# Optimization experiments

Hardware: AMD Instinct MI355X
Metric: run time of the kernel (lower is better)

The kernel has to match this reference:

```python
import jax, jax.numpy as jnp
import numpy as np

X_DIM, Z_DIM, H, B, T = 257, 16, 128, 256, 512


def _p(key, shape, scale=0.05):
    return jax.random.normal(key, shape, jnp.float32) * scale


def setup_inputs() -> dict:
    key = jax.random.key(0)
    ks = jax.random.split(key, 16)
    z4 = jnp.zeros((4 * H,), jnp.float32)
    return {
        "x": jax.random.uniform(ks[0], (B, X_DIM, T), jnp.float32),
        "eps": jax.random.normal(ks[1], (T, B, Z_DIM), jnp.float32),
        # rnn_g_x: backward LSTM over x
        "Wih_gx": _p(ks[2], (4 * H, X_DIM)), "Whh_gx": _p(ks[3], (4 * H, H)),
        "bih_gx": z4, "bhh_gx": z4,
        # rnn_g_z: forward LSTM cell over sampled z
        "Wih_gz": _p(ks[4], (4 * H, Z_DIM)), "Whh_gz": _p(ks[5], (4 * H, H)),
        "bih_gz": z4, "bhh_gz": z4,
        # mlp_inference (one dense layer, tanh) + heads
        "W0": _p(ks[6], (H, 2 * H)), "b0": jnp.zeros((H,), jnp.float32),
        "Wm": _p(ks[7], (Z_DIM, H)), "bm": jnp.zeros((Z_DIM,), jnp.float32),
        "Wv": _p(ks[8], (Z_DIM, H)), "bv": jnp.zeros((Z_DIM,), jnp.float32),
        # decoder rnn_h + gen_logvar
        "Wih_h": _p(ks[9], (4 * H, Z_DIM)), "Whh_h": _p(ks[10], (4 * H, H)),
        "bih_h": z4, "bhh_h": z4,
        "Wy": _p(ks[11], (X_DIM, H)), "by": jnp.zeros((X_DIM,), jnp.float32),
    }


def _lstm(xs, Wih, Whh, b, reverse=False):
    # xs: (T, B, in); single-layer LSTM, PyTorch gate order i,f,g,o
    Bn, Hd = xs.shape[1], Whh.shape[1]

    def step(carry, x_t):
        h, c = carry
        g = x_t @ Wih.T + h @ Whh.T + b
        i, f, gg, o = jnp.split(g, 4, axis=-1)
        c = jax.nn.sigmoid(f) * c + jax.nn.sigmoid(i) * jnp.tanh(gg)
        h = jax.nn.sigmoid(o) * jnp.tanh(c)
        return (h, c), h

    init = (jnp.zeros((Bn, Hd), xs.dtype), jnp.zeros((Bn, Hd), xs.dtype))
    _, hs = jax.lax.scan(step, init, xs, reverse=reverse)
    return hs


def reference(x, eps, Wih_gx, Whh_gx, bih_gx, bhh_gx,
              Wih_gz, Whh_gz, bih_gz, bhh_gz,
              W0, b0, Wm, bm, Wv, bv,
              Wih_h, Whh_h, bih_h, bhh_h, Wy, by):
    xt = jnp.transpose(x, (2, 0, 1))  # (T, B, x_dim)
    # g_x = flip(LSTM(flip(x))) == backward-direction LSTM
    g_x = _lstm(xt, Wih_gx, Whh_gx, bih_gx + bhh_gx, reverse=True)
    bz = bih_gz + bhh_gz
    Hz = Whh_gz.shape[1]

    def inf_step(carry, inp):
        g_z, c_z = carry  # hidden of rnn_g_z BEFORE seeing current z
        gx_t, eps_t = inp
        h = jnp.tanh(jnp.concatenate([gx_t, g_z], axis=-1) @ W0.T + b0)
        mean = h @ Wm.T + bm
        logvar = h @ Wv.T + bv
        z_t = eps_t * jnp.exp(0.5 * logvar) + mean  # reparameterize
        # one LSTM-cell step of rnn_g_z on z_t (used at next timestep)
        g = z_t @ Wih_gz.T + g_z @ Whh_gz.T + bz
        i, f, gg, o = jnp.split(g, 4, axis=-1)
        c_z = jax.nn.sigmoid(f) * c_z + jax.nn.sigmoid(i) * jnp.tanh(gg)
        g_z = jax.nn.sigmoid(o) * jnp.tanh(c_z)
        return (g_z, c_z), (mean, logvar, z_t)

    Bn = xt.shape[1]
    init = (jnp.zeros((Bn, Hz), x.dtype), jnp.zeros((Bn, Hz), x.dtype))
    _, (mean, logvar, z) = jax.lax.scan(inf_step, init, (g_x, eps))
    # generation
    hdec = _lstm(z, Wih_h, Whh_h, bih_h + bhh_h)
    y = jnp.exp(hdec @ Wy.T + by)  # (T, B, x_dim)
    perm = lambda a: jnp.transpose(a, (1, 2, 0))  # -> (B, dim, T)
    return perm(y), perm(mean), perm(logvar), perm(z)
```

## Files before the change

kernel.cpp:

```cpp
#include <hip/hip_runtime.h>
#include <stdint.h>

#define T_SEQ 512
#define BATCH 256
#define HID   128
#define G4    512
#define XD    257
#define ZD    16

__device__ __forceinline__ float bf2f(uint16_t u) {
  union { uint32_t i; float f; } v; v.i = ((uint32_t)u) << 16; return v.f;
}
__device__ __forceinline__ uint16_t f2bf(float f) {
  union { float f; uint32_t i; } v; v.f = f;
  uint32_t r = v.i + 0x7fffu + ((v.i >> 16) & 1u);
  return (uint16_t)(r >> 16);
}
__device__ __forceinline__ float tanhfast(float x) { return 2.0f / (1.0f + __expf(-2.0f * x)) - 1.0f; }
__device__ __forceinline__ float gate_act(float pre, bool isg) {
  float s = isg ? (-2.0f * pre) : (-pre);
  float r = 1.0f / (1.0f + __expf(s));
  return isg ? (2.0f * r - 1.0f) : r;
}

#define PIN(x) asm volatile("" : "+v"(x))

template <int C>
__device__ __forceinline__ float dppq(float x) {
  return __int_as_float(__builtin_amdgcn_mov_dpp(__float_as_int(x), C, 0xF, 0xF, true));
}
template <int O>
__device__ __forceinline__ float swzx(float x) {
  return __int_as_float(__builtin_amdgcn_ds_swizzle(__float_as_int(x), O));
}

__device__ __forceinline__ float quad_reduce4(float a0, float a1, float a2, float a3, int g) {
  bool lb = (g & 1) != 0;
  float rl = dppq<0xB1>(lb ? a0 : a1);
  float rh = dppq<0xB1>(lb ? a2 : a3);
  float bl = (lb ? a1 : a0) + rl;
  float bh = (lb ? a3 : a2) + rh;
  bool hb = (g & 2) != 0;
  float r2 = dppq<0x4E>(hb ? bl : bh);
  return (hb ? bh : bl) + r2;
}

__global__ void k_prep(const float* __restrict__ Wih_gx, const float* __restrict__ Wy,
                       float* __restrict__ wT, float* __restrict__ wyT) {
  int idx = blockIdx.x * 256 + threadIdx.x;
  const int N1 = XD * G4;
  const int N2 = HID * XD;
  if (idx < N1) {
    int j = idx & (G4 - 1), d = idx >> 9;
    wT[idx] = Wih_gx[j * XD + d];
  } else if (idx < N1 + N2) {
    int i2 = idx - N1;
    int u = i2 / XD, d = i2 % XD;
    wyT[i2] = Wy[d * HID + u];
  }
}

__global__ __launch_bounds__(256) void k_proj(
    const float* __restrict__ x, const float* __restrict__ wT,
    const float* __restrict__ bih, const float* __restrict__ bhh,
    uint16_t* __restrict__ px) {
  __shared__ uint16_t xs[XD * 66];
  int tid = threadIdx.x;
  int t0 = blockIdx.x * 64, b = blockIdx.y;
  int lane = tid & 63;
  {
    int t = tid & 63, d0 = tid >> 6;
    for (int d = d0; d < XD; d += 4)
      xs[d * 66 + t] = f2bf(x[((size_t)b * XD + d) * T_SEQ + t0 + t]);
  }
  __syncthreads();
  int w = __builtin_amdgcn_readfirstlane(tid >> 6);
  for (int p = 0; p < 8; ++p) {
    int j0 = w * 128 + p * 16;
    float acc[16];
#pragma unroll
    for (int i = 0; i < 16; ++i) acc[i] = bih[j0 + i] + bhh[j0 + i];
    for (int d = 0; d < XD; ++d) {
      float xv = bf2f(xs[d * 66 + lane]);
      const float* wrow = wT + (size_t)d * G4 + j0;
#pragma unroll
      for (int i = 0; i < 16; ++i) acc[i] = fmaf(wrow[i], xv, acc[i]);
    }
    size_t base = ((size_t)(t0 + lane) * BATCH + b) * G4 + j0;
    uint32_t pk[8];
#pragma unroll
    for (int i = 0; i < 8; ++i)
      pk[i] = (uint32_t)f2bf(acc[2 * i]) | ((uint32_t)f2bf(acc[2 * i + 1]) << 16);
    uint4* dst = (uint4*)(px + base);
    dst[0] = make_uint4(pk[0], pk[1], pk[2], pk[3]);
    dst[1] = make_uint4(pk[4], pk[5], pk[6], pk[7]);
  }
}

__global__ __launch_bounds__(512, 1) void k_lstm_gx(
    const uint16_t* __restrict__ px, const float* __restrict__ Whh,
    uint16_t* __restrict__ gx) {
  __shared__ __align__(128) float hl[2][HID];
  int tid = threadIdx.x, b = blockIdx.x;
  int u = tid >> 2, g = tid & 3;
  int j = g * HID + u;
  int rot = g << 1, hbase = g << 3;
  float wA[4][32];
#pragma unroll
  for (int q = 0; q < 4; ++q)
#pragma unroll
    for (int n = 0; n < 8; ++n) {
      int i = n ^ rot;
      float4 wv = *(const float4*)(Whh + ((size_t)(q * HID + u)) * HID + g * 32 + i * 4);
      wA[q][4 * n + 0] = wv.x; wA[q][4 * n + 1] = wv.y;
      wA[q][4 * n + 2] = wv.z; wA[q][4 * n + 3] = wv.w;
    }
#pragma unroll
  for (int q = 0; q < 4; ++q)
#pragma unroll
    for (int i = 0; i < 32; ++i) PIN(wA[q][i]);
  if (tid < HID) hl[0][tid] = 0.0f;
  float c = 0.0f;
  int cur = 0;
  bool isg = (g == 2);
  uint16_t pcur = px[((size_t)(T_SEQ - 1) * BATCH + b) * G4 + j];
  __syncthreads();
  for (int t = T_SEQ - 1; t >= 0; --t) {
    int tn = t > 0 ? t - 1 : 0;
    uint16_t pnext = px[((size_t)tn * BATCH + b) * G4 + j];
    const float4* h4 = (const float4*)hl[cur];
    float a0 = 0.f, a1 = 0.f, a2 = 0.f, a3 = 0.f;
#pragma unroll
    for (int n = 0; n < 8; ++n) {
      float4 hv = h4[hbase + (n ^ rot)];
      a0 = fmaf(wA[0][4 * n + 0], hv.x, a0); a0 = fmaf(wA[0][4 * n + 1], hv.y, a0);
      a0 = fmaf(wA[0][4 * n + 2], hv.z, a0); a0 = fmaf(wA[0][4 * n + 3], hv.w, a0);
      a1 = fmaf(wA[1][4 * n + 0], hv.x, a1); a1 = fmaf(wA[1][4 * n + 1], hv.y, a1);
      a1 = fmaf(wA[1][4 * n + 2], hv.z, a1); a1 = fmaf(wA[1][4 * n + 3], hv.w, a1);
      a2 = fmaf(wA[2][4 * n + 0], hv.x, a2); a2 = fmaf(wA[2][4 * n + 1], hv.y, a2);
      a2 = fmaf(wA[2][4 * n + 2], hv.z, a2); a2 = fmaf(wA[2][4 * n + 3], hv.w, a2);
      a3 = fmaf(wA[3][4 * n + 0], hv.x, a3); a3 = fmaf(wA[3][4 * n + 1], hv.y, a3);
      a3 = fmaf(wA[3][4 * n + 2], hv.z, a3); a3 = fmaf(wA[3][4 * n + 3], hv.w, a3);
    }
    float pre = quad_reduce4(a0, a1, a2, a3, g) + bf2f(pcur);
    float act = gate_act(pre, isg);
    float af = dppq<0x55>(act);
    float ag = dppq<0xAA>(act);
    float ao = dppq<0xFF>(act);
    if (g == 0) {
      c = af * c + act * ag;
      float h = ao * tanhfast(c);
      hl[cur ^ 1][u] = h;
      gx[((size_t)t * BATCH + b) * HID + u] = f2bf(h);
    }
    cur ^= 1;
    pcur = pnext;
    __syncthreads();
  }
}

__global__ __launch_bounds__(512, 1) void k_inf(
    const uint16_t* __restrict__ gx, const float* __restrict__ eps,
    const float* __restrict__ Wih_gz, const float* __restrict__ Whh_gz,
    const float* __restrict__ bih_gz, const float* __restrict__ bhh_gz,
    const float* __restrict__ W0, const float* __restrict__ b0,
    const float* __restrict__ Wm, const float* __restrict__ bm,
    const float* __restrict__ Wv, const float* __restrict__ bv,
    float* __restrict__ zbuf, float* __restrict__ out_mean,
    float* __restrict__ out_logvar, float* __restrict__ out_z) {
  __shared__ __align__(128) float gxl[HID];
  __shared__ __align__(128) float gzl[2][HID];
  __shared__ __align__(128) float hvec[16 * 12];
  __shared__ __align__(128) float zl[ZD];
  int tid = threadIdx.x, b = blockIdx.x;
  int u = tid >> 2, g = tid & 3;
  int j = g * HID + u;
  int rot = g << 1, hbase = g << 3;
  float wA[4][32];
  float4 wz[4];
#pragma unroll
  for (int q = 0; q < 4; ++q) {
#pragma unroll
    for (int n = 0; n < 8; ++n) {
      int i = n ^ rot;
      float4 wv = *(const float4*)(Whh_gz + ((size_t)(q * HID + u)) * HID + g * 32 + i * 4);
      wA[q][4 * n + 0] = wv.x; wA[q][4 * n + 1] = wv.y;
      wA[q][4 * n + 2] = wv.z; wA[q][4 * n + 3] = wv.w;
    }
    wz[q] = *(const float4*)(Wih_gz + (size_t)(q * HID + u) * ZD + g * 4);
  }
#pragma unroll
  for (int q = 0; q < 4; ++q) {
#pragma unroll
    for (int i = 0; i < 32; ++i) PIN(wA[q][i]);
    PIN(wz[q].x); PIN(wz[q].y); PIN(wz[q].z); PIN(wz[q].w);
  }
  float bzr = bih_gz[j] + bhh_gz[j];
  int sB = tid & 7, uB = (tid >> 3) << 1;
  float w0a[32], w0b[32];
#pragma unroll
  for (int n = 0; n < 8; ++n) {
    int i = n ^ sB;
    float4 va = *(const float4*)(W0 + (size_t)uB * 256 + sB * 32 + i * 4);
    float4 vb = *(const float4*)(W0 + (size_t)(uB + 1) * 256 + sB * 32 + i * 4);
    w0a[4 * n + 0] = va.x; w0a[4 * n + 1] = va.y; w0a[4 * n + 2] = va.z; w0a[4 * n + 3] = va.w;
    w0b[4 * n + 0] = vb.x; w0b[4 * n + 1] = vb.y; w0b[4 * n + 2] = vb.z; w0b[4 * n + 3] = vb.w;
  }
#pragma unroll
  for (int i = 0; i < 32; ++i) { PIN(w0a[i]); PIN(w0b[i]); }
  float b0a = b0[uB], b0b = b0[uB + 1];
  int o = tid >> 5, lo = tid & 31;
  float wmr[8];
  {
    const float* Wsel = (lo < 16) ? (Wm + (size_t)o * HID + (lo & 15) * 8)
                                  : (Wv + (size_t)o * HID + (lo & 15) * 8);
#pragma unroll
    for (int i = 0; i < 8; ++i) wmr[i] = Wsel[i];
  }
  float bmr = bm[o], bvr = bv[o];
  float czr = 0.0f;
  int cur = 0;
  bool isg = (g == 2);
  if (tid < HID) {
    gzl[0][tid] = 0.0f;
    gxl[tid] = bf2f(gx[(size_t)b * HID + tid]);
  }
  float epcur = (lo == 0) ? eps[(size_t)b * ZD + o] : 0.0f;
  __syncthreads();
  for (int t = 0; t < T_SEQ; ++t) {
    int tn = (t < T_SEQ - 1) ? t + 1 : t;
    float gxnext = (tid < HID) ? bf2f(gx[((size_t)tn * BATCH + b) * HID + tid]) : 0.0f;
    float epnext = (lo == 0) ? eps[((size_t)tn * BATCH + b) * ZD + o] : 0.0f;
    {
      const float4* seg = (sB < 4) ? ((const float4*)gxl + (sB << 3))
                                   : ((const float4*)(gzl[cur]) + ((sB - 4) << 3));
      float pa = 0.f, pb = 0.f;
#pragma unroll
      for (int n = 0; n < 8; ++n) {
        float4 v = seg[n ^ sB];
        pa = fmaf(w0a[4 * n + 0], v.x, pa); pa = fmaf(w0a[4 * n + 1], v.y, pa);
        pa = fmaf(w0a[4 * n + 2], v.z, pa); pa = fmaf(w0a[4 * n + 3], v.w, pa);
        pb = fmaf(w0b[4 * n + 0], v.x, pb); pb = fmaf(w0b[4 * n + 1], v.y, pb);
        pb = fmaf(w0b[4 * n + 2], v.z, pb); pb = fmaf(w0b[4 * n + 3], v.w, pb);
      }
      pa += dppq<0xB1>(pa); pa += dppq<0x4E>(pa); pa += swzx<0x101F>(pa);
      pb += dppq<0xB1>(pb); pb += dppq<0x4E>(pb); pb += swzx<0x101F>(pb);
      if (sB == 0) {
        hvec[((uB >> 3) * 12) + (uB & 7)] = tanhfast(pa + b0a);
        int u1 = uB + 1;
        hvec[((u1 >> 3) * 12) + (u1 & 7)] = tanhfast(pb + b0b);
      }
    }
    __syncthreads();
    {
      int m = lo & 15;
      const float4* hh = (const float4*)(hvec + m * 12);
      float4 h0 = hh[0], h1 = hh[1];
      float p = wmr[0] * h0.x + wmr[1] * h0.y + wmr[2] * h0.z + wmr[3] * h0.w +
                wmr[4] * h1.x + wmr[5] * h1.y + wmr[6] * h1.z + wmr[7] * h1.w;
      p += dppq<0xB1>(p);
      p += dppq<0x4E>(p);
      p += swzx<0x101F>(p);
      p += swzx<0x201F>(p);
      float other = swzx<0x401F>(p);
      if (lo == 0) {
        float mean = p + bmr;
        float lv = other + bvr;
        float zv = epcur * __expf(0.5f * lv) + mean;
        zl[o] = zv;
        out_mean[((size_t)b * ZD + o) * T_SEQ + t] = mean;
        out_logvar[((size_t)b * ZD + o) * T_SEQ + t] = lv;
        out_z[((size_t)b * ZD + o) * T_SEQ + t] = zv;
        zbuf[((size_t)t * BATCH + b) * ZD + o] = zv;
      }
    }
    __syncthreads();
    {
      float4 zv = ((const float4*)zl)[g];
      float a0 = wz[0].x * zv.x; a0 = fmaf(wz[0].y, zv.y, a0);
      a0 = fmaf(wz[0].z, zv.z, a0); a0 = fmaf(wz[0].w, zv.w, a0);
      float a1 = wz[1].x * zv.x; a1 = fmaf(wz[1].y, zv.y, a1);
      a1 = fmaf(wz[1].z, zv.z, a1); a1 = fmaf(wz[1].w, zv.w, a1);
      float a2 = wz[2].x * zv.x; a2 = fmaf(wz[2].y, zv.y, a2);
      a2 = fmaf(wz[2].z, zv.z, a2); a2 = fmaf(wz[2].w, zv.w, a2);
      float a3 = wz[3].x * zv.x; a3 = fmaf(wz[3].y, zv.y, a3);
      a3 = fmaf(wz[3].z, zv.z, a3); a3 = fmaf(wz[3].w, zv.w, a3);
      const float4* h4 = (const float4*)gzl[cur];
#pragma unroll
      for (int n = 0; n < 8; ++n) {
        float4 hv = h4[hbase + (n ^ rot)];
        a0 = fmaf(wA[0][4 * n + 0], hv.x, a0); a0 = fmaf(wA[0][4 * n + 1], hv.y, a0);
        a0 = fmaf(wA[0][4 * n + 2], hv.z, a0); a0 = fmaf(wA[0][4 * n + 3], hv.w, a0);
        a1 = fmaf(wA[1][4 * n + 0], hv.x, a1); a1 = fmaf(wA[1][4 * n + 1], hv.y, a1);
        a1 = fmaf(wA[1][4 * n + 2], hv.z, a1); a1 = fmaf(wA[1][4 * n + 3], hv.w, a1);
        a2 = fmaf(wA[2][4 * n + 0], hv.x, a2); a2 = fmaf(wA[2][4 * n + 1], hv.y, a2);
        a2 = fmaf(wA[2][4 * n + 2], hv.z, a2); a2 = fmaf(wA[2][4 * n + 3], hv.w, a2);
        a3 = fmaf(wA[3][4 * n + 0], hv.x, a3); a3 = fmaf(wA[3][4 * n + 1], hv.y, a3);
        a3 = fmaf(wA[3][4 * n + 2], hv.z, a3); a3 = fmaf(wA[3][4 * n + 3], hv.w, a3);
      }
      float pre = quad_reduce4(a0, a1, a2, a3, g) + bzr;
      float act = gate_act(pre, isg);
      float af = dppq<0x55>(act);
      float ag = dppq<0xAA>(act);
      float ao = dppq<0xFF>(act);
      if (g == 0) {
        czr = af * czr + act * ag;
        gzl[cur ^ 1][u] = ao * tanhfast(czr);
      }
      if (tid < HID) gxl[tid] = gxnext;
    }
    epcur = epnext;
    cur ^= 1;
    __syncthreads();
  }
}

__global__ __launch_bounds__(512, 1) void k_dec(
    const float* __restrict__ zbuf, const float* __restrict__ Wih_h,
    const float* __restrict__ Whh_h, const float* __restrict__ bih,
    const float* __restrict__ bhh, uint16_t* __restrict__ hdec) {
  __shared__ __align__(128) float hl[2][HID];
  __shared__ __align__(128) float zls[2][ZD];
  int tid = threadIdx.x, b = blockIdx.x;
  int u = tid >> 2, g = tid & 3;
  int j = g * HID + u;
  int rot = g << 1, hbase = g << 3;
  float wA[4][32];
  float4 wz[4];
#pragma unroll
  for (int q = 0; q < 4; ++q) {
#pragma unroll
    for (int n = 0; n < 8; ++n) {
      int i = n ^ rot;
      float4 wv = *(const float4*)(Whh_h + ((size_t)(q * HID + u)) * HID + g * 32 + i * 4);
      wA[q][4 * n + 0] = wv.x; wA[q][4 * n + 1] = wv.y;
      wA[q][4 * n + 2] = wv.z; wA[q][4 * n + 3] = wv.w;
    }
    wz[q] = *(const float4*)(Wih_h + (size_t)(q * HID + u) * ZD + g * 4);
  }
#pragma unroll
  for (int q = 0; q < 4; ++q) {
#pragma unroll
    for (int i = 0; i < 32; ++i) PIN(wA[q][i]);
    PIN(wz[q].x); PIN(wz[q].y); PIN(wz[q].z); PIN(wz[q].w);
  }
  float bz = bih[j] + bhh[j];
  if (tid < HID) hl[0][tid] = 0.0f;
  if (tid < ZD) zls[0][tid] = zbuf[(size_t)b * ZD + tid];
  float c = 0.0f;
  int cur = 0;
  bool isg = (g == 2);
  __syncthreads();
  for (int t = 0; t < T_SEQ; ++t) {
    int tn = (t < T_SEQ - 1) ? t + 1 : t;
    float znext = (tid < ZD) ? zbuf[((size_t)tn * BATCH + b) * ZD + tid] : 0.0f;
    float4 zv = ((const float4*)zls[cur])[g];
    float a0 = wz[0].x * zv.x; a0 = fmaf(wz[0].y, zv.y, a0);
    a0 = fmaf(wz[0].z, zv.z, a0); a0 = fmaf(wz[0].w, zv.w, a0);
    float a1 = wz[1].x * zv.x; a1 = fmaf(wz[1].y, zv.y, a1);
    a1 = fmaf(wz[1].z, zv.z, a1); a1 = fmaf(wz[1].w, zv.w, a1);
    float a2 = wz[2].x * zv.x; a2 = fmaf(wz[2].y, zv.y, a2);
    a2 = fmaf(wz[2].z, zv.z, a2); a2 = fmaf(wz[2].w, zv.w, a2);
    float a3 = wz[3].x * zv.x; a3 = fmaf(wz[3].y, zv.y, a3);
    a3 = fmaf(wz[3].z, zv.z, a3); a3 = fmaf(wz[3].w, zv.w, a3);
    const float4* h4 = (const float4*)hl[cur];
#pragma unroll
    for (int n = 0; n < 8; ++n) {
      float4 hv = h4[hbase + (n ^ rot)];
      a0 = fmaf(wA[0][4 * n + 0], hv.x, a0); a0 = fmaf(wA[0][4 * n + 1], hv.y, a0);
      a0 = fmaf(wA[0][4 * n + 2], hv.z, a0); a0 = fmaf(wA[0][4 * n + 3], hv.w, a0);
      a1 = fmaf(wA[1][4 * n + 0], hv.x, a1); a1 = fmaf(wA[1][4 * n + 1], hv.y, a1);
      a1 = fmaf(wA[1][4 * n + 2], hv.z, a1); a1 = fmaf(wA[1][4 * n + 3], hv.w, a1);
      a2 = fmaf(wA[2][4 * n + 0], hv.x, a2); a2 = fmaf(wA[2][4 * n + 1], hv.y, a2);
      a2 = fmaf(wA[2][4 * n + 2], hv.z, a2); a2 = fmaf(wA[2][4 * n + 3], hv.w, a2);
      a3 = fmaf(wA[3][4 * n + 0], hv.x, a3); a3 = fmaf(wA[3][4 * n + 1], hv.y, a3);
      a3 = fmaf(wA[3][4 * n + 2], hv.z, a3); a3 = fmaf(wA[3][4 * n + 3], hv.w, a3);
    }
    float pre = quad_reduce4(a0, a1, a2, a3, g) + bz;
    float act = gate_act(pre, isg);
    float af = dppq<0x55>(act);
    float ag = dppq<0xAA>(act);
    float ao = dppq<0xFF>(act);
    if (g == 0) {
      c = af * c + act * ag;
      float h = ao * tanhfast(c);
      hl[cur ^ 1][u] = h;
      hdec[((size_t)t * BATCH + b) * HID + u] = f2bf(h);
    }
    if (tid < ZD) zls[cur ^ 1][tid] = znext;
    cur ^= 1;
    __syncthreads();
  }
}

__global__ __launch_bounds__(256) void k_y(
    const uint16_t* __restrict__ hdec, const float* __restrict__ wyT,
    const float* __restrict__ by, float* __restrict__ out_y) {
  __shared__ __align__(16) float hl[HID * 65];
  int tid = threadIdx.x;
  int t0 = blockIdx.x * 64, b = blockIdx.y;
  {
    int uu = tid & 127, tg = tid >> 7;
    for (int tt = tg; tt < 64; tt += 2)
      hl[uu * 65 + tt] = bf2f(hdec[((size_t)(t0 + tt) * BATCH + b) * HID + uu]);
  }
  __syncthreads();
  int w = __builtin_amdgcn_readfirstlane(tid >> 6);
  int lane = tid & 63;
  for (int p = 0; p < 4; ++p) {
    int d0 = w * 16 + p * 64;
    float acc[16];
#pragma unroll
    for (int i = 0; i < 16; ++i) acc[i] = by[d0 + i];
    for (int uu = 0; uu < HID; ++uu) {
      float hv = hl[uu * 65 + lane];
      const float* wrow = wyT + (size_t)uu * XD + d0;
#pragma unroll
      for (int i = 0; i < 16; ++i) acc[i] = fmaf(wrow[i], hv, acc[i]);
    }
#pragma unroll
    for (int i = 0; i < 16; ++i)
      out_y[((size_t)b * XD + d0 + i) * T_SEQ + t0 + lane] = __expf(acc[i]);
  }
  if (w == 0) {
    float acc = by[256];
    for (int uu = 0; uu < HID; ++uu)
      acc = fmaf(wyT[(size_t)uu * XD + 256], hl[uu * 65 + lane], acc);
    out_y[((size_t)b * XD + 256) * T_SEQ + t0 + lane] = __expf(acc);
  }
}

extern "C" void kernel_launch(void* const* d_in, const int* in_sizes, int n_in,
                              void* d_out, int out_size, void* d_ws, size_t ws_size,
                              hipStream_t stream) {
  const float* x      = (const float*)d_in[0];
  const float* eps    = (const float*)d_in[1];
  const float* Wih_gx = (const float*)d_in[2];
  const float* Whh_gx = (const float*)d_in[3];
  const float* bih_gx = (const float*)d_in[4];
  const float* bhh_gx = (const float*)d_in[5];
  const float* Wih_gz = (const float*)d_in[6];
  const float* Whh_gz = (const float*)d_in[7];
  const float* bih_gz = (const float*)d_in[8];
  const float* bhh_gz = (const float*)d_in[9];
  const float* W0     = (const float*)d_in[10];
  const float* b0     = (const float*)d_in[11];
  const float* Wm     = (const float*)d_in[12];
  const float* bm     = (const float*)d_in[13];
  const float* Wv     = (const float*)d_in[14];
  const float* bv     = (const float*)d_in[15];
  const float* Wih_h  = (const float*)d_in[16];
  const float* Whh_h  = (const float*)d_in[17];
  const float* bih_h  = (const float*)d_in[18];
  const float* bhh_h  = (const float*)d_in[19];
  const float* Wy     = (const float*)d_in[20];
  const float* by     = (const float*)d_in[21];

  char* ws = (char*)d_ws;
  float*    wT   = (float*)(ws + 0);
  float*    wyT  = (float*)(ws + 526336);
  uint16_t* px   = (uint16_t*)(ws + (1u << 20));
  uint16_t* gx   = (uint16_t*)(ws + 135266304);
  float*    zbuf = (float*)(ws + 168820736);
  uint16_t* hdec = (uint16_t*)(ws + 177209344);

  float* out_y      = (float*)d_out;
  float* out_mean   = out_y + (size_t)BATCH * XD * T_SEQ;
  float* out_logvar = out_mean + (size_t)BATCH * ZD * T_SEQ;
  float* out_z      = out_logvar + (size_t)BATCH * ZD * T_SEQ;

  k_prep<<<dim3(643), dim3(256), 0, stream>>>(Wih_gx, Wy, wT, wyT);
  k_proj<<<dim3(8, 256), dim3(256), 0, stream>>>(x, wT, bih_gx, bhh_gx, px);
  k_lstm_gx<<<dim3(256), dim3(512), 0, stream>>>(px, Whh_gx, gx);
  k_inf<<<dim3(256), dim3(512), 0, stream>>>(gx, eps, Wih_gz, Whh_gz, bih_gz, bhh_gz,
                                             W0, b0, Wm, bm, Wv, bv,
                                             zbuf, out_mean, out_logvar, out_z);
  k_dec<<<dim3(256), dim3(512), 0, stream>>>(zbuf, Wih_h, Whh_h, bih_h, bhh_h, hdec);
  k_y<<<dim3(8, 256), dim3(256), 0, stream>>>(hdec, wyT, by, out_y);
}
```

Measured before the change: 3.429 ms.

## Split each LSTM gate row across 8 lanes with 1024-thread blocks

```diff
diff --git a/kernel.cpp b/kernel.cpp
--- a/kernel.cpp
+++ b/kernel.cpp
@@ -97,28 +97,27 @@
   }
 }
 
-__global__ __launch_bounds__(512, 1) void k_lstm_gx(
+__global__ __launch_bounds__(1024) void k_lstm_gx(
     const uint16_t* __restrict__ px, const float* __restrict__ Whh,
     uint16_t* __restrict__ gx) {
   __shared__ __align__(128) float hl[2][HID];
   int tid = threadIdx.x, b = blockIdx.x;
-  int u = tid >> 2, g = tid & 3;
+  int u = tid >> 3, s = tid & 7, g = s & 3;
   int j = g * HID + u;
-  int rot = g << 1, hbase = g << 3;
-  float wA[4][32];
+  float wA[4][16];
 #pragma unroll
   for (int q = 0; q < 4; ++q)
 #pragma unroll
-    for (int n = 0; n < 8; ++n) {
-      int i = n ^ rot;
-      float4 wv = *(const float4*)(Whh + ((size_t)(q * HID + u)) * HID + g * 32 + i * 4);
+    for (int n = 0; n < 4; ++n) {
+      int p = (n + s) & 3;
+      float4 wv = *(const float4*)(Whh + ((size_t)(q * HID + u)) * HID + s * 16 + p * 4);
       wA[q][4 * n + 0] = wv.x; wA[q][4 * n + 1] = wv.y;
       wA[q][4 * n + 2] = wv.z; wA[q][4 * n + 3] = wv.w;
     }
 #pragma unroll
   for (int q = 0; q < 4; ++q)
 #pragma unroll
-    for (int i = 0; i < 32; ++i) PIN(wA[q][i]);
+    for (int i = 0; i < 16; ++i) PIN(wA[q][i]);
   if (tid < HID) hl[0][tid] = 0.0f;
   float c = 0.0f;
   int cur = 0;
@@ -131,8 +130,8 @@
     const float4* h4 = (const float4*)hl[cur];
     float a0 = 0.f, a1 = 0.f, a2 = 0.f, a3 = 0.f;
 #pragma unroll
-    for (int n = 0; n < 8; ++n) {
-      float4 hv = h4[hbase + (n ^ rot)];
+    for (int n = 0; n < 4; ++n) {
+      float4 hv = h4[s * 4 + ((n + s) & 3)];
       a0 = fmaf(wA[0][4 * n + 0], hv.x, a0); a0 = fmaf(wA[0][4 * n + 1], hv.y, a0);
       a0 = fmaf(wA[0][4 * n + 2], hv.z, a0); a0 = fmaf(wA[0][4 * n + 3], hv.w, a0);
       a1 = fmaf(wA[1][4 * n + 0], hv.x, a1); a1 = fmaf(wA[1][4 * n + 1], hv.y, a1);
@@ -142,7 +141,9 @@
       a3 = fmaf(wA[3][4 * n + 0], hv.x, a3); a3 = fmaf(wA[3][4 * n + 1], hv.y, a3);
       a3 = fmaf(wA[3][4 * n + 2], hv.z, a3); a3 = fmaf(wA[3][4 * n + 3], hv.w, a3);
     }
-    float pre = quad_reduce4(a0, a1, a2, a3, g) + bf2f(pcur);
+    float pre = quad_reduce4(a0, a1, a2, a3, g);
+    pre += swzx<0x101F>(pre);
+    pre += bf2f(pcur);
     float act = gate_act(pre, isg);
     float af = dppq<0x55>(act);
     float ag = dppq<0xAA>(act);
@@ -150,8 +151,10 @@
     if (g == 0) {
       c = af * c + act * ag;
       float h = ao * tanhfast(c);
-      hl[cur ^ 1][u] = h;
-      gx[((size_t)t * BATCH + b) * HID + u] = f2bf(h);
+      if (s == 0) {
+        hl[cur ^ 1][u] = h;
+        gx[((size_t)t * BATCH + b) * HID + u] = f2bf(h);
+      }
     }
     cur ^= 1;
     pcur = pnext;
@@ -159,7 +162,7 @@
   }
 }
 
-__global__ __launch_bounds__(512, 1) void k_inf(
+__global__ __launch_bounds__(1024) void k_inf(
     const uint16_t* __restrict__ gx, const float* __restrict__ eps,
     const float* __restrict__ Wih_gz, const float* __restrict__ Whh_gz,
     const float* __restrict__ bih_gz, const float* __restrict__ bhh_gz,
@@ -173,51 +176,51 @@
   __shared__ __align__(128) float hvec[16 * 12];
   __shared__ __align__(128) float zl[ZD];
   int tid = threadIdx.x, b = blockIdx.x;
-  int u = tid >> 2, g = tid & 3;
+  int u = tid >> 3, s = tid & 7, g = s & 3;
   int j = g * HID + u;
-  int rot = g << 1, hbase = g << 3;
-  float wA[4][32];
-  float4 wz[4];
+  float wA[4][16];
+  float2 wz[4];
 #pragma unroll
   for (int q = 0; q < 4; ++q) {
 #pragma unroll
-    for (int n = 0; n < 8; ++n) {
-      int i = n ^ rot;
-      float4 wv = *(const float4*)(Whh_gz + ((size_t)(q * HID + u)) * HID + g * 32 + i * 4);
+    for (int n = 0; n < 4; ++n) {
+      int p = (n + s) & 3;
+      float4 wv = *(const float4*)(Whh_gz + ((size_t)(q * HID + u)) * HID + s * 16 + p * 4);
       wA[q][4 * n + 0] = wv.x; wA[q][4 * n + 1] = wv.y;
       wA[q][4 * n + 2] = wv.z; wA[q][4 * n + 3] = wv.w;
     }
-    wz[q] = *(const float4*)(Wih_gz + (size_t)(q * HID + u) * ZD + g * 4);
+    wz[q] = *(const float2*)(Wih_gz + (size_t)(q * HID + u) * ZD + s * 2);
   }
 #pragma unroll
   for (int q = 0; q < 4; ++q) {
 #pragma unroll
-    for (int i = 0; i < 32; ++i) PIN(wA[q][i]);
-    PIN(wz[q].x); PIN(wz[q].y); PIN(wz[q].z); PIN(wz[q].w);
+    for (int i = 0; i < 16; ++i) PIN(wA[q][i]);
+    PIN(wz[q].x); PIN(wz[q].y);
   }
   float bzr = bih_gz[j] + bhh_gz[j];
-  int sB = tid & 7, uB = (tid >> 3) << 1;
-  float w0a[32], w0b[32];
+  float w0r[32];
 #pragma unroll
   for (int n = 0; n < 8; ++n) {
-    int i = n ^ sB;
-    float4 va = *(const float4*)(W0 + (size_t)uB * 256 + sB * 32 + i * 4);
-    float4 vb = *(const float4*)(W0 + (size_t)(uB + 1) * 256 + sB * 32 + i * 4);
-    w0a[4 * n + 0] = va.x; w0a[4 * n + 1] = va.y; w0a[4 * n + 2] = va.z; w0a[4 * n + 3] = va.w;
-    w0b[4 * n + 0] = vb.x; w0b[4 * n + 1] = vb.y; w0b[4 * n + 2] = vb.z; w0b[4 * n + 3] = vb.w;
-  }
-#pragma unroll
-  for (int i = 0; i < 32; ++i) { PIN(w0a[i]); PIN(w0b[i]); }
-  float b0a = b0[uB], b0b = b0[uB + 1];
-  int o = tid >> 5, lo = tid & 31;
-  float wmr[8];
-  {
+    int p = (n + s) & 7;
+    float4 va = *(const float4*)(W0 + (size_t)u * 256 + s * 32 + p * 4);
+    w0r[4 * n + 0] = va.x; w0r[4 * n + 1] = va.y;
+    w0r[4 * n + 2] = va.z; w0r[4 * n + 3] = va.w;
+  }
+#pragma unroll
+  for (int i = 0; i < 32; ++i) PIN(w0r[i]);
+  float b0r = b0[u];
+  bool loC = tid < 512;
+  int o = (tid >> 5) & 15, lo = tid & 31;
+  float wmr[8] = {0, 0, 0, 0, 0, 0, 0, 0};
+  float bmr = 0.f, bvr = 0.f, epcur = 0.f;
+  if (loC) {
     const float* Wsel = (lo < 16) ? (Wm + (size_t)o * HID + (lo & 15) * 8)
                                   : (Wv + (size_t)o * HID + (lo & 15) * 8);
 #pragma unroll
     for (int i = 0; i < 8; ++i) wmr[i] = Wsel[i];
-  }
-  float bmr = bm[o], bvr = bv[o];
+    bmr = bm[o]; bvr = bv[o];
+    if (lo == 0) epcur = eps[(size_t)b * ZD + o];
+  }
   float czr = 0.0f;
   int cur = 0;
   bool isg = (g == 2);
@@ -225,34 +228,26 @@
     gzl[0][tid] = 0.0f;
     gxl[tid] = bf2f(gx[(size_t)b * HID + tid]);
   }
-  float epcur = (lo == 0) ? eps[(size_t)b * ZD + o] : 0.0f;
   __syncthreads();
   for (int t = 0; t < T_SEQ; ++t) {
     int tn = (t < T_SEQ - 1) ? t + 1 : t;
     float gxnext = (tid < HID) ? bf2f(gx[((size_t)tn * BATCH + b) * HID + tid]) : 0.0f;
-    float epnext = (lo == 0) ? eps[((size_t)tn * BATCH + b) * ZD + o] : 0.0f;
+    float epnext = (loC && lo == 0) ? eps[((size_t)tn * BATCH + b) * ZD + o] : 0.0f;
     {
-      const float4* seg = (sB < 4) ? ((const float4*)gxl + (sB << 3))
-                                   : ((const float4*)(gzl[cur]) + ((sB - 4) << 3));
-      float pa = 0.f, pb = 0.f;
+      const float4* seg = (s < 4) ? ((const float4*)gxl + s * 8)
+                                  : ((const float4*)(gzl[cur]) + (s - 4) * 8);
+      float pa = 0.f;
 #pragma unroll
       for (int n = 0; n < 8; ++n) {
-        float4 v = seg[n ^ sB];
-        pa = fmaf(w0a[4 * n + 0], v.x, pa); pa = fmaf(w0a[4 * n + 1], v.y, pa);
-        pa = fmaf(w0a[4 * n + 2], v.z, pa); pa = fmaf(w0a[4 * n + 3], v.w, pa);
-        pb = fmaf(w0b[4 * n + 0], v.x, pb); pb = fmaf(w0b[4 * n + 1], v.y, pb);
-        pb = fmaf(w0b[4 * n + 2], v.z, pb); pb = fmaf(w0b[4 * n + 3], v.w, pb);
+        float4 v = seg[(n + s) & 7];
+        pa = fmaf(w0r[4 * n + 0], v.x, pa); pa = fmaf(w0r[4 * n + 1], v.y, pa);
+        pa = fmaf(w0r[4 * n + 2], v.z, pa); pa = fmaf(w0r[4 * n + 3], v.w, pa);
       }
       pa += dppq<0xB1>(pa); pa += dppq<0x4E>(pa); pa += swzx<0x101F>(pa);
-      pb += dppq<0xB1>(pb); pb += dppq<0x4E>(pb); pb += swzx<0x101F>(pb);
-      if (sB == 0) {
-        hvec[((uB >> 3) * 12) + (uB & 7)] = tanhfast(pa + b0a);
-        int u1 = uB + 1;
-        hvec[((u1 >> 3) * 12) + (u1 & 7)] = tanhfast(pb + b0b);
-      }
+      if (s == 0) hvec[(u >> 3) * 12 + (u & 7)] = tanhfast(pa + b0r);
     }
     __syncthreads();
-    {
+    if (loC) {
       int m = lo & 15;
       const float4* hh = (const float4*)(hvec + m * 12);
       float4 h0 = hh[0], h1 = hh[1];
@@ -276,19 +271,15 @@
     }
     __syncthreads();
     {
-      float4 zv = ((const float4*)zl)[g];
-      float a0 = wz[0].x * zv.x; a0 = fmaf(wz[0].y, zv.y, a0);
-      a0 = fmaf(wz[0].z, zv.z, a0); a0 = fmaf(wz[0].w, zv.w, a0);
-      float a1 = wz[1].x * zv.x; a1 = fmaf(wz[1].y, zv.y, a1);
-      a1 = fmaf(wz[1].z, zv.z, a1); a1 = fmaf(wz[1].w, zv.w, a1);
-      float a2 = wz[2].x * zv.x; a2 = fmaf(wz[2].y, zv.y, a2);
-      a2 = fmaf(wz[2].z, zv.z, a2); a2 = fmaf(wz[2].w, zv.w, a2);
-      float a3 = wz[3].x * zv.x; a3 = fmaf(wz[3].y, zv.y, a3);
-      a3 = fmaf(wz[3].z, zv.z, a3); a3 = fmaf(wz[3].w, zv.w, a3);
+      float2 zz = *(const float2*)(zl + s * 2);
+      float a0 = fmaf(wz[0].y, zz.y, wz[0].x * zz.x);
+      float a1 = fmaf(wz[1].y, zz.y, wz[1].x * zz.x);
+      float a2 = fmaf(wz[2].y, zz.y, wz[2].x * zz.x);
+      float a3 = fmaf(wz[3].y, zz.y, wz[3].x * zz.x);
       const float4* h4 = (const float4*)gzl[cur];
 #pragma unroll
-      for (int n = 0; n < 8; ++n) {
-        float4 hv = h4[hbase + (n ^ rot)];
+      for (int n = 0; n < 4; ++n) {
+        float4 hv = h4[s * 4 + ((n + s) & 3)];
         a0 = fmaf(wA[0][4 * n + 0], hv.x, a0); a0 = fmaf(wA[0][4 * n + 1], hv.y, a0);
         a0 = fmaf(wA[0][4 * n + 2], hv.z, a0); a0 = fmaf(wA[0][4 * n + 3], hv.w, a0);
         a1 = fmaf(wA[1][4 * n + 0], hv.x, a1); a1 = fmaf(wA[1][4 * n + 1], hv.y, a1);
@@ -298,14 +289,17 @@
         a3 = fmaf(wA[3][4 * n + 0], hv.x, a3); a3 = fmaf(wA[3][4 * n + 1], hv.y, a3);
         a3 = fmaf(wA[3][4 * n + 2], hv.z, a3); a3 = fmaf(wA[3][4 * n + 3], hv.w, a3);
       }
-      float pre = quad_reduce4(a0, a1, a2, a3, g) + bzr;
+      float pre = quad_reduce4(a0, a1, a2, a3, g);
+      pre += swzx<0x101F>(pre);
+      pre += bzr;
       float act = gate_act(pre, isg);
       float af = dppq<0x55>(act);
       float ag = dppq<0xAA>(act);
       float ao = dppq<0xFF>(act);
       if (g == 0) {
         czr = af * czr + act * ag;
-        gzl[cur ^ 1][u] = ao * tanhfast(czr);
+        float h = ao * tanhfast(czr);
+        if (s == 0) gzl[cur ^ 1][u] = h;
       }
       if (tid < HID) gxl[tid] = gxnext;
     }
@@ -315,34 +309,33 @@
   }
 }
 
-__global__ __launch_bounds__(512, 1) void k_dec(
+__global__ __launch_bounds__(1024) void k_dec(
     const float* __restrict__ zbuf, const float* __restrict__ Wih_h,
     const float* __restrict__ Whh_h, const float* __restrict__ bih,
     const float* __restrict__ bhh, uint16_t* __restrict__ hdec) {
   __shared__ __align__(128) float hl[2][HID];
   __shared__ __align__(128) float zls[2][ZD];
   int tid = threadIdx.x, b = blockIdx.x;
-  int u = tid >> 2, g = tid & 3;
+  int u = tid >> 3, s = tid & 7, g = s & 3;
   int j = g * HID + u;
-  int rot = g << 1, hbase = g << 3;
-  float wA[4][32];
-  float4 wz[4];
+  float wA[4][16];
+  float2 wz[4];
 #pragma unroll
   for (int q = 0; q < 4; ++q) {
 #pragma unroll
-    for (int n = 0; n < 8; ++n) {
-      int i = n ^ rot;
-      float4 wv = *(const float4*)(Whh_h + ((size_t)(q * HID + u)) * HID + g * 32 + i * 4);
+    for (int n = 0; n < 4; ++n) {
+      int p = (n + s) & 3;
+      float4 wv = *(const float4*)(Whh_h + ((size_t)(q * HID + u)) * HID + s * 16 + p * 4);
       wA[q][4 * n + 0] = wv.x; wA[q][4 * n + 1] = wv.y;
       wA[q][4 * n + 2] = wv.z; wA[q][4 * n + 3] = wv.w;
     }
-    wz[q] = *(const float4*)(Wih_h + (size_t)(q * HID + u) * ZD + g * 4);
+    wz[q] = *(const float2*)(Wih_h + (size_t)(q * HID + u) * ZD + s * 2);
   }
 #pragma unroll
   for (int q = 0; q < 4; ++q) {
 #pragma unroll
-    for (int i = 0; i < 32; ++i) PIN(wA[q][i]);
-    PIN(wz[q].x); PIN(wz[q].y); PIN(wz[q].z); PIN(wz[q].w);
+    for (int i = 0; i < 16; ++i) PIN(wA[q][i]);
+    PIN(wz[q].x); PIN(wz[q].y);
   }
   float bz = bih[j] + bhh[j];
   if (tid < HID) hl[0][tid] = 0.0f;
@@ -354,19 +347,15 @@
   for (int t = 0; t < T_SEQ; ++t) {
     int tn = (t < T_SEQ - 1) ? t + 1 : t;
     float znext = (tid < ZD) ? zbuf[((size_t)tn * BATCH + b) * ZD + tid] : 0.0f;
-    float4 zv = ((const float4*)zls[cur])[g];
-    float a0 = wz[0].x * zv.x; a0 = fmaf(wz[0].y, zv.y, a0);
-    a0 = fmaf(wz[0].z, zv.z, a0); a0 = fmaf(wz[0].w, zv.w, a0);
-    float a1 = wz[1].x * zv.x; a1 = fmaf(wz[1].y, zv.y, a1);
-    a1 = fmaf(wz[1].z, zv.z, a1); a1 = fmaf(wz[1].w, zv.w, a1);
-    float a2 = wz[2].x * zv.x; a2 = fmaf(wz[2].y, zv.y, a2);
-    a2 = fmaf(wz[2].z, zv.z, a2); a2 = fmaf(wz[2].w, zv.w, a2);
-    float a3 = wz[3].x * zv.x; a3 = fmaf(wz[3].y, zv.y, a3);
-    a3 = fmaf(wz[3].z, zv.z, a3); a3 = fmaf(wz[3].w, zv.w, a3);
+    float2 zz = *(const float2*)(zls[cur] + s * 2);
+    float a0 = fmaf(wz[0].y, zz.y, wz[0].x * zz.x);
+    float a1 = fmaf(wz[1].y, zz.y, wz[1].x * zz.x);
+    float a2 = fmaf(wz[2].y, zz.y, wz[2].x * zz.x);
+    float a3 = fmaf(wz[3].y, zz.y, wz[3].x * zz.x);
     const float4* h4 = (const float4*)hl[cur];
 #pragma unroll
-    for (int n = 0; n < 8; ++n) {
-      float4 hv = h4[hbase + (n ^ rot)];
+    for (int n = 0; n < 4; ++n) {
+      float4 hv = h4[s * 4 + ((n + s) & 3)];
       a0 = fmaf(wA[0][4 * n + 0], hv.x, a0); a0 = fmaf(wA[0][4 * n + 1], hv.y, a0);
       a0 = fmaf(wA[0][4 * n + 2], hv.z, a0); a0 = fmaf(wA[0][4 * n + 3], hv.w, a0);
       a1 = fmaf(wA[1][4 * n + 0], hv.x, a1); a1 = fmaf(wA[1][4 * n + 1], hv.y, a1);
@@ -376,7 +365,9 @@
       a3 = fmaf(wA[3][4 * n + 0], hv.x, a3); a3 = fmaf(wA[3][4 * n + 1], hv.y, a3);
       a3 = fmaf(wA[3][4 * n + 2], hv.z, a3); a3 = fmaf(wA[3][4 * n + 3], hv.w, a3);
     }
-    float pre = quad_reduce4(a0, a1, a2, a3, g) + bz;
+    float pre = quad_reduce4(a0, a1, a2, a3, g);
+    pre += swzx<0x101F>(pre);
+    pre += bz;
     float act = gate_act(pre, isg);
     float af = dppq<0x55>(act);
     float ag = dppq<0xAA>(act);
@@ -384,8 +375,10 @@
     if (g == 0) {
       c = af * c + act * ag;
       float h = ao * tanhfast(c);
-      hl[cur ^ 1][u] = h;
-      hdec[((size_t)t * BATCH + b) * HID + u] = f2bf(h);
+      if (s == 0) {
+        hl[cur ^ 1][u] = h;
+        hdec[((size_t)t * BATCH + b) * HID + u] = f2bf(h);
+      }
     }
     if (tid < ZD) zls[cur ^ 1][tid] = znext;
     cur ^= 1;
@@ -471,10 +464,10 @@
 
   k_prep<<<dim3(643), dim3(256), 0, stream>>>(Wih_gx, Wy, wT, wyT);
   k_proj<<<dim3(8, 256), dim3(256), 0, stream>>>(x, wT, bih_gx, bhh_gx, px);
-  k_lstm_gx<<<dim3(256), dim3(512), 0, stream>>>(px, Whh_gx, gx);
-  k_inf<<<dim3(256), dim3(512), 0, stream>>>(gx, eps, Wih_gz, Whh_gz, bih_gz, bhh_gz,
-                                             W0, b0, Wm, bm, Wv, bv,
-                                             zbuf, out_mean, out_logvar, out_z);
-  k_dec<<<dim3(256), dim3(512), 0, stream>>>(zbuf, Wih_h, Whh_h, bih_h, bhh_h, hdec);
+  k_lstm_gx<<<dim3(256), dim3(1024), 0, stream>>>(px, Whh_gx, gx);
+  k_inf<<<dim3(256), dim3(1024), 0, stream>>>(gx, eps, Wih_gz, Whh_gz, bih_gz, bhh_gz,
+                                              W0, b0, Wm, bm, Wv, bv,
+                                              zbuf, out_mean, out_logvar, out_z);
+  k_dec<<<dim3(256), dim3(1024), 0, stream>>>(zbuf, Wih_h, Whh_h, bih_h, bhh_h, hdec);
   k_y<<<dim3(8, 256), dim3(256), 0, stream>>>(hdec, wyT, by, out_y);
 }
```

New measurement: 5.946 ms. 1.73x slower.

## Move half of recurrent LSTM weights to LDS to cut register pressure

Applied to the files above, without the earlier changes.

```diff
diff --git a/kernel.cpp b/kernel.cpp
--- a/kernel.cpp
+++ b/kernel.cpp
@@ -97,17 +97,18 @@
   }
 }
 
-__global__ __launch_bounds__(512, 1) void k_lstm_gx(
+__global__ __launch_bounds__(512) void k_lstm_gx(
     const uint16_t* __restrict__ px, const float* __restrict__ Whh,
     uint16_t* __restrict__ gx) {
+  __shared__ float4 wl[16][512];
   __shared__ __align__(128) float hl[2][HID];
   int tid = threadIdx.x, b = blockIdx.x;
   int u = tid >> 2, g = tid & 3;
   int j = g * HID + u;
   int rot = g << 1, hbase = g << 3;
-  float wA[4][32];
-#pragma unroll
-  for (int q = 0; q < 4; ++q)
+  float wA[2][32];
+#pragma unroll
+  for (int q = 0; q < 2; ++q)
 #pragma unroll
     for (int n = 0; n < 8; ++n) {
       int i = n ^ rot;
@@ -116,9 +117,15 @@
       wA[q][4 * n + 2] = wv.z; wA[q][4 * n + 3] = wv.w;
     }
 #pragma unroll
-  for (int q = 0; q < 4; ++q)
+  for (int q = 0; q < 2; ++q)
 #pragma unroll
     for (int i = 0; i < 32; ++i) PIN(wA[q][i]);
+#pragma unroll
+  for (int n = 0; n < 8; ++n) {
+    int i = n ^ rot;
+    wl[n][tid]     = *(const float4*)(Whh + ((size_t)(2 * HID + u)) * HID + g * 32 + i * 4);
+    wl[8 + n][tid] = *(const float4*)(Whh + ((size_t)(3 * HID + u)) * HID + g * 32 + i * 4);
+  }
   if (tid < HID) hl[0][tid] = 0.0f;
   float c = 0.0f;
   int cur = 0;
@@ -133,14 +140,16 @@
 #pragma unroll
     for (int n = 0; n < 8; ++n) {
       float4 hv = h4[hbase + (n ^ rot)];
+      float4 w2 = wl[n][tid];
+      float4 w3 = wl[8 + n][tid];
       a0 = fmaf(wA[0][4 * n + 0], hv.x, a0); a0 = fmaf(wA[0][4 * n + 1], hv.y, a0);
       a0 = fmaf(wA[0][4 * n + 2], hv.z, a0); a0 = fmaf(wA[0][4 * n + 3], hv.w, a0);
       a1 = fmaf(wA[1][4 * n + 0], hv.x, a1); a1 = fmaf(wA[1][4 * n + 1], hv.y, a1);
       a1 = fmaf(wA[1][4 * n + 2], hv.z, a1); a1 = fmaf(wA[1][4 * n + 3], hv.w, a1);
-      a2 = fmaf(wA[2][4 * n + 0], hv.x, a2); a2 = fmaf(wA[2][4 * n + 1], hv.y, a2);
-      a2 = fmaf(wA[2][4 * n + 2], hv.z, a2); a2 = fmaf(wA[2][4 * n + 3], hv.w, a2);
-      a3 = fmaf(wA[3][4 * n + 0], hv.x, a3); a3 = fmaf(wA[3][4 * n + 1], hv.y, a3);
-      a3 = fmaf(wA[3][4 * n + 2], hv.z, a3); a3 = fmaf(wA[3][4 * n + 3], hv.w, a3);
+      a2 = fmaf(w2.x, hv.x, a2); a2 = fmaf(w2.y, hv.y, a2);
+      a2 = fmaf(w2.z, hv.z, a2); a2 = fmaf(w2.w, hv.w, a2);
+      a3 = fmaf(w3.x, hv.x, a3); a3 = fmaf(w3.y, hv.y, a3);
+      a3 = fmaf(w3.z, hv.z, a3); a3 = fmaf(w3.w, hv.w, a3);
     }
     float pre = quad_reduce4(a0, a1, a2, a3, g) + bf2f(pcur);
     float act = gate_act(pre, isg);
@@ -159,7 +168,7 @@
   }
 }
 
-__global__ __launch_bounds__(512, 1) void k_inf(
+__global__ __launch_bounds__(512) void k_inf(
     const uint16_t* __restrict__ gx, const float* __restrict__ eps,
     const float* __restrict__ Wih_gz, const float* __restrict__ Whh_gz,
     const float* __restrict__ bih_gz, const float* __restrict__ bhh_gz,
@@ -168,6 +177,7 @@
     const float* __restrict__ Wv, const float* __restrict__ bv,
     float* __restrict__ zbuf, float* __restrict__ out_mean,
     float* __restrict__ out_logvar, float* __restrict__ out_z) {
+  __shared__ float4 wl[16][512];
   __shared__ __align__(128) float gxl[HID];
   __shared__ __align__(128) float gzl[2][HID];
   __shared__ __align__(128) float hvec[16 * 12];
@@ -176,10 +186,10 @@
   int u = tid >> 2, g = tid & 3;
   int j = g * HID + u;
   int rot = g << 1, hbase = g << 3;
-  float wA[4][32];
+  float wA[2][32];
   float4 wz[4];
 #pragma unroll
-  for (int q = 0; q < 4; ++q) {
+  for (int q = 0; q < 2; ++q)
 #pragma unroll
     for (int n = 0; n < 8; ++n) {
       int i = n ^ rot;
@@ -187,27 +197,25 @@
       wA[q][4 * n + 0] = wv.x; wA[q][4 * n + 1] = wv.y;
       wA[q][4 * n + 2] = wv.z; wA[q][4 * n + 3] = wv.w;
     }
+#pragma unroll
+  for (int q = 0; q < 4; ++q)
     wz[q] = *(const float4*)(Wih_gz + (size_t)(q * HID + u) * ZD + g * 4);
-  }
-#pragma unroll
-  for (int q = 0; q < 4; ++q) {
+#pragma unroll
+  for (int q = 0; q < 2; ++q)
 #pragma unroll
     for (int i = 0; i < 32; ++i) PIN(wA[q][i]);
-    PIN(wz[q].x); PIN(wz[q].y); PIN(wz[q].z); PIN(wz[q].w);
+#pragma unroll
+  for (int q = 0; q < 4; ++q) { PIN(wz[q].x); PIN(wz[q].y); PIN(wz[q].z); PIN(wz[q].w); }
+#pragma unroll
+  for (int n = 0; n < 8; ++n) {
+    int i = n ^ rot;
+    wl[n][tid]     = *(const float4*)(Whh_gz + ((size_t)(2 * HID + u)) * HID + g * 32 + i * 4);
+    wl[8 + n][tid] = *(const float4*)(Whh_gz + ((size_t)(3 * HID + u)) * HID + g * 32 + i * 4);
   }
   float bzr = bih_gz[j] + bhh_gz[j];
   int sB = tid & 7, uB = (tid >> 3) << 1;
-  float w0a[32], w0b[32];
-#pragma unroll
-  for (int n = 0; n < 8; ++n) {
-    int i = n ^ sB;
-    float4 va = *(const float4*)(W0 + (size_t)uB * 256 + sB * 32 + i * 4);
-    float4 vb = *(const float4*)(W0 + (size_t)(uB + 1) * 256 + sB * 32 + i * 4);
-    w0a[4 * n + 0] = va.x; w0a[4 * n + 1] = va.y; w0a[4 * n + 2] = va.z; w0a[4 * n + 3] = va.w;
-    w0b[4 * n + 0] = vb.x; w0b[4 * n + 1] = vb.y; w0b[4 * n + 2] = vb.z; w0b[4 * n + 3] = vb.w;
-  }
-#pragma unroll
-  for (int i = 0; i < 32; ++i) { PIN(w0a[i]); PIN(w0b[i]); }
+  uintptr_t w0pa_u = (uintptr_t)(W0 + (size_t)uB * 256 + sB * 32);
+  uintptr_t w0pb_u = (uintptr_t)(W0 + (size_t)(uB + 1) * 256 + sB * 32);
   float b0a = b0[uB], b0b = b0[uB + 1];
   int o = tid >> 5, lo = tid & 31;
   float wmr[8];
@@ -217,6 +225,8 @@
 #pragma unroll
     for (int i = 0; i < 8; ++i) wmr[i] = Wsel[i];
   }
+#pragma unroll
+  for (int i = 0; i < 8; ++i) PIN(wmr[i]);
   float bmr = bm[o], bvr = bv[o];
   float czr = 0.0f;
   int cur = 0;
@@ -232,16 +242,22 @@
     float gxnext = (tid < HID) ? bf2f(gx[((size_t)tn * BATCH + b) * HID + tid]) : 0.0f;
     float epnext = (lo == 0) ? eps[((size_t)tn * BATCH + b) * ZD + o] : 0.0f;
     {
+      asm volatile("" : "+v"(w0pa_u), "+v"(w0pb_u));
+      const float4* w0pa = (const float4*)w0pa_u;
+      const float4* w0pb = (const float4*)w0pb_u;
       const float4* seg = (sB < 4) ? ((const float4*)gxl + (sB << 3))
                                    : ((const float4*)(gzl[cur]) + ((sB - 4) << 3));
       float pa = 0.f, pb = 0.f;
 #pragma unroll
       for (int n = 0; n < 8; ++n) {
-        float4 v = seg[n ^ sB];
-        pa = fmaf(w0a[4 * n + 0], v.x, pa); pa = fmaf(w0a[4 * n + 1], v.y, pa);
-        pa = fmaf(w0a[4 * n + 2], v.z, pa); pa = fmaf(w0a[4 * n + 3], v.w, pa);
-        pb = fmaf(w0b[4 * n + 0], v.x, pb); pb = fmaf(w0b[4 * n + 1], v.y, pb);
-        pb = fmaf(w0b[4 * n + 2], v.z, pb); pb = fmaf(w0b[4 * n + 3], v.w, pb);
+        int i = n ^ sB;
+        float4 v = seg[i];
+        float4 wa = w0pa[i];
+        float4 wb = w0pb[i];
+        pa = fmaf(wa.x, v.x, pa); pa = fmaf(wa.y, v.y, pa);
+        pa = fmaf(wa.z, v.z, pa); pa = fmaf(wa.w, v.w, pa);
+        pb = fmaf(wb.x, v.x, pb); pb = fmaf(wb.y, v.y, pb);
+        pb = fmaf(wb.z, v.z, pb); pb = fmaf(wb.w, v.w, pb);
       }
       pa += dppq<0xB1>(pa); pa += dppq<0x4E>(pa); pa += swzx<0x101F>(pa);
       pb += dppq<0xB1>(pb); pb += dppq<0x4E>(pb); pb += swzx<0x101F>(pb);
@@ -289,14 +305,16 @@
 #pragma unroll
       for (int n = 0; n < 8; ++n) {
         float4 hv = h4[hbase + (n ^ rot)];
+        float4 w2 = wl[n][tid];
+        float4 w3 = wl[8 + n][tid];
         a0 = fmaf(wA[0][4 * n + 0], hv.x, a0); a0 = fmaf(wA[0][4 * n + 1], hv.y, a0);
         a0 = fmaf(wA[0][4 * n + 2], hv.z, a0); a0 = fmaf(wA[0][4 * n + 3], hv.w, a0);
         a1 = fmaf(wA[1][4 * n + 0], hv.x, a1); a1 = fmaf(wA[1][4 * n + 1], hv.y, a1);
         a1 = fmaf(wA[1][4 * n + 2], hv.z, a1); a1 = fmaf(wA[1][4 * n + 3], hv.w, a1);
-        a2 = fmaf(wA[2][4 * n + 0], hv.x, a2); a2 = fmaf(wA[2][4 * n + 1], hv.y, a2);
-        a2 = fmaf(wA[2][4 * n + 2], hv.z, a2); a2 = fmaf(wA[2][4 * n + 3], hv.w, a2);
-        a3 = fmaf(wA[3][4 * n + 0], hv.x, a3); a3 = fmaf(wA[3][4 * n + 1], hv.y, a3);
-        a3 = fmaf(wA[3][4 * n + 2], hv.z, a3); a3 = fmaf(wA[3][4 * n + 3], hv.w, a3);
+        a2 = fmaf(w2.x, hv.x, a2); a2 = fmaf(w2.y, hv.y, a2);
+        a2 = fmaf(w2.z, hv.z, a2); a2 = fmaf(w2.w, hv.w, a2);
+        a3 = fmaf(w3.x, hv.x, a3); a3 = fmaf(w3.y, hv.y, a3);
+        a3 = fmaf(w3.z, hv.z, a3); a3 = fmaf(w3.w, hv.w, a3);
       }
       float pre = quad_reduce4(a0, a1, a2, a3, g) + bzr;
       float act = gate_act(pre, isg);
@@ -315,20 +333,21 @@
   }
 }
 
-__global__ __launch_bounds__(512, 1) void k_dec(
+__global__ __launch_bounds__(512) void k_dec(
     const float* __restrict__ zbuf, const float* __restrict__ Wih_h,
     const float* __restrict__ Whh_h, const float* __restrict__ bih,
     const float* __restrict__ bhh, uint16_t* __restrict__ hdec) {
+  __shared__ float4 wl[16][512];
   __shared__ __align__(128) float hl[2][HID];
   __shared__ __align__(128) float zls[2][ZD];
   int tid = threadIdx.x, b = blockIdx.x;
   int u = tid >> 2, g = tid & 3;
   int j = g * HID + u;
   int rot = g << 1, hbase = g << 3;
-  float wA[4][32];
+  float wA[2][32];
   float4 wz[4];
 #pragma unroll
-  for (int q = 0; q < 4; ++q) {
+  for (int q = 0; q < 2; ++q)
 #pragma unroll
     for (int n = 0; n < 8; ++n) {
       int i = n ^ rot;
@@ -336,13 +355,20 @@
       wA[q][4 * n + 0] = wv.x; wA[q][4 * n + 1] = wv.y;
       wA[q][4 * n + 2] = wv.z; wA[q][4 * n + 3] = wv.w;
     }
+#pragma unroll
+  for (int q = 0; q < 4; ++q)
     wz[q] = *(const float4*)(Wih_h + (size_t)(q * HID + u) * ZD + g * 4);
-  }
-#pragma unroll
-  for (int q = 0; q < 4; ++q) {
+#pragma unroll
+  for (int q = 0; q < 2; ++q)
 #pragma unroll
     for (int i = 0; i < 32; ++i) PIN(wA[q][i]);
-    PIN(wz[q].x); PIN(wz[q].y); PIN(wz[q].z); PIN(wz[q].w);
+#pragma unroll
+  for (int q = 0; q < 4; ++q) { PIN(wz[q].x); PIN(wz[q].y); PIN(wz[q].z); PIN(wz[q].w); }
+#pragma unroll
+  for (int n = 0; n < 8; ++n) {
+    int i = n ^ rot;
+    wl[n][tid]     = *(const float4*)(Whh_h + ((size_t)(2 * HID + u)) * HID + g * 32 + i * 4);
+    wl[8 + n][tid] = *(const float4*)(Whh_h + ((size_t)(3 * HID + u)) * HID + g * 32 + i * 4);
   }
   float bz = bih[j] + bhh[j];
   if (tid < HID) hl[0][tid] = 0.0f;
@@ -367,14 +393,16 @@
 #pragma unroll
     for (int n = 0; n < 8; ++n) {
       float4 hv = h4[hbase + (n ^ rot)];
+      float4 w2 = wl[n][tid];
+      float4 w3 = wl[8 + n][tid];
       a0 = fmaf(wA[0][4 * n + 0], hv.x, a0); a0 = fmaf(wA[0][4 * n + 1], hv.y, a0);
       a0 = fmaf(wA[0][4 * n + 2], hv.z, a0); a0 = fmaf(wA[0][4 * n + 3], hv.w, a0);
       a1 = fmaf(wA[1][4 * n + 0], hv.x, a1); a1 = fmaf(wA[1][4 * n + 1], hv.y, a1);
       a1 = fmaf(wA[1][4 * n + 2], hv.z, a1); a1 = fmaf(wA[1][4 * n + 3], hv.w, a1);
-      a2 = fmaf(wA[2][4 * n + 0], hv.x, a2); a2 = fmaf(wA[2][4 * n + 1], hv.y, a2);
-      a2 = fmaf(wA[2][4 * n + 2], hv.z, a2); a2 = fmaf(wA[2][4 * n + 3], hv.w, a2);
-      a3 = fmaf(wA[3][4 * n + 0], hv.x, a3); a3 = fmaf(wA[3][4 * n + 1], hv.y, a3);
-      a3 = fmaf(wA[3][4 * n + 2], hv.z, a3); a3 = fmaf(wA[3][4 * n + 3], hv.w, a3);
+      a2 = fmaf(w2.x, hv.x, a2); a2 = fmaf(w2.y, hv.y, a2);
+      a2 = fmaf(w2.z, hv.z, a2); a2 = fmaf(w2.w, hv.w, a2);
+      a3 = fmaf(w3.x, hv.x, a3); a3 = fmaf(w3.y, hv.y, a3);
+      a3 = fmaf(w3.z, hv.z, a3); a3 = fmaf(w3.w, hv.w, a3);
     }
     float pre = quad_reduce4(a0, a1, a2, a3, g) + bz;
     float act = gate_act(pre, isg);
```

New measurement: 6.669 ms. 1.94x slower.
